# Performance work log

Measured on AMD Instinct MI355X. Metric: run time of the kernel, lower is better.

Reference implementation:

```python
import jax, jax.numpy as jnp
import numpy as np

B, D, N = 2, 256, 8192   # batch, in_channels, sequence length
CI = 128                 # inter_channels
BN_EPS = 1e-5


def conv1x1(w, b, x):
    # w: (Cout, Cin), b: (Cout,), x: (B, Cin, N) -> (B, Cout, N)
    return jnp.einsum('oc,bcn->bon', w, x) + b[None, :, None]


def maxpool2(x):
    # MaxPool1d(kernel_size=2): (B, C, N) -> (B, C, N//2)
    b, c, n = x.shape
    return x.reshape(b, c, n // 2, 2).max(axis=-1)


def setup_inputs() -> dict:
    key = jax.random.key(0)
    ks = jax.random.split(key, 11)
    s_in = 1.0 / np.sqrt(D)
    s_ci = 1.0 / np.sqrt(CI)
    return {
        'f': jax.random.normal(ks[0], (B, D, N), dtype=jnp.float32),
        'g_w': jax.random.uniform(ks[1], (CI, D), jnp.float32, -s_in, s_in),
        'g_b': jax.random.uniform(ks[2], (CI,), jnp.float32, -s_in, s_in),
        'theta_w': jax.random.uniform(ks[3], (CI, D), jnp.float32, -s_in, s_in),
        'theta_b': jax.random.uniform(ks[4], (CI,), jnp.float32, -s_in, s_in),
        'phi_w': jax.random.uniform(ks[5], (CI, D), jnp.float32, -s_in, s_in),
        'phi_b': jax.random.uniform(ks[6], (CI,), jnp.float32, -s_in, s_in),
        'W_w': jax.random.uniform(ks[7], (D, CI), jnp.float32, -s_ci, s_ci),
        'W_b': jax.random.uniform(ks[8], (D,), jnp.float32, -s_ci, s_ci),
        'bn_gamma': jax.random.normal(ks[9], (D,), dtype=jnp.float32) * 0.1,
        'bn_beta': jax.random.normal(ks[10], (D,), dtype=jnp.float32) * 0.1,
    }


def reference(f, g_w, g_b, theta_w, theta_b, phi_w, phi_b, W_w, W_b, bn_gamma, bn_beta):
    # projections (1x1 convs); g and phi are sub-sampled by maxpool(2)
    g_f = maxpool2(conv1x1(g_w, g_b, f))          # (B, CI, N/2)
    theta_f = conv1x1(theta_w, theta_b, f)        # (B, CI, N)
    phi_f = maxpool2(conv1x1(phi_w, phi_b, f))    # (B, CI, N/2)

    # affinity: theta^T @ phi, softmax over keys (no scale, as in source)
    A = jnp.einsum('bcn,bcm->bnm', theta_f, phi_f)     # (B, N, N/2)
    A = jax.nn.softmax(A, axis=-1)
    y = jnp.einsum('bnm,bcm->bcn', A, g_f)             # (B, CI, N)

    # W: 1x1 conv + BatchNorm1d (training-mode batch stats), residual
    Wy = conv1x1(W_w, W_b, y)                          # (B, D, N)
    mean = Wy.mean(axis=(0, 2), keepdims=True)
    var = Wy.var(axis=(0, 2), keepdims=True)           # biased, like torch BN
    Wy = (Wy - mean) * jax.lax.rsqrt(var + BN_EPS)
    Wy = Wy * bn_gamma[None, :, None] + bn_beta[None, :, None]
    return Wy + f
```

## Files before the change

### kernel.cpp

```cpp
#include <hip/hip_runtime.h>
#include <hip/hip_bf16.h>
#include <math.h>

#define B_ 2
#define D_ 256
#define N_ 8192
#define CI_ 128
#define M_ 4096
#define BN_EPS_ 1e-5f
#define LOG2E_ 1.4426950408889634f

#define GLOBAL_AS __attribute__((address_space(1)))
#define LDS_AS __attribute__((address_space(3)))

#define OFF_WALL 0
#define OFF_THT  65536
#define OFF_PHT  (OFF_THT + 1048576)
#define OFF_GT   (OFF_PHT + 524288)
#define OFF_YP   (OFF_GT  + 524288)
#define OFF_ML   (OFF_YP  + 4194304)
#define OFF_MEAN (OFF_ML + 131072)
#define OFF_RSTD (OFF_MEAN + 256)

typedef __attribute__((ext_vector_type(8))) short bfrag;
typedef __attribute__((ext_vector_type(4))) float f4v;
typedef __attribute__((ext_vector_type(16))) float f16v;
typedef __attribute__((ext_vector_type(4))) short s4v;
typedef __attribute__((ext_vector_type(4))) unsigned u4v;

__device__ inline unsigned short bf16rne(float x) {
    unsigned u = __float_as_uint(x);
    u += 0x7fff + ((u >> 16) & 1);
    return (unsigned short)(u >> 16);
}

__device__ inline float exp2fast(float x) {
    float r;
    asm("v_exp_f32 %0, %1" : "=v"(r) : "v"(x));
    return r;
}

__global__ __launch_bounds__(256) void wconv_kernel(
    const float* __restrict__ gw, const float* __restrict__ tw, const float* __restrict__ pw,
    const float* __restrict__ Ww, short* __restrict__ wall)
{
    int idx = blockIdx.x * 256 + threadIdx.x;
    int which = idx >> 15;
    int rem = idx & 32767;
    const float* src = (which == 0) ? gw : (which == 1) ? tw : (which == 2) ? pw : Ww;
    float v = src[rem];
    if (which == 1) v *= LOG2E_;
    wall[idx] = (short)bf16rne(v);
}

__global__ __launch_bounds__(256, 2) void proj_kernel(
    const float* __restrict__ f, const short* __restrict__ wall,
    const float* __restrict__ tb, const float* __restrict__ gb, const float* __restrict__ pb,
    short* __restrict__ th_t, short* __restrict__ g_t, short* __restrict__ ph_t)
{
    __shared__ short sF[32 * 72];

    const int tid = threadIdx.x;
    const int wave = tid >> 6, lane = tid & 63;
    const int lq = lane & 15, quad = lane >> 4;
    const int b = blockIdx.y;
    const int n0 = blockIdx.x * 32;

    const float* fb = f + (size_t)b * D_ * N_;

    f4v acc[6][2];
#pragma unroll
    for (int ct = 0; ct < 6; ct++)
#pragma unroll
        for (int nf = 0; nf < 2; nf++) acc[ct][nf] = (f4v){0.f, 0.f, 0.f, 0.f};

    const int sn = tid & 31;
    const int sgrp = tid >> 5;

    for (int kc = 0; kc < D_; kc += 64) {
        __syncthreads();
#pragma unroll
        for (int jj = 0; jj < 4; jj++) {
            int dd = kc + sgrp * 8 + 2 * jj;
            float v0 = fb[(size_t)dd * N_ + n0 + sn];
            float v1 = fb[(size_t)(dd + 1) * N_ + n0 + sn];
            unsigned pk = (unsigned)bf16rne(v0) | ((unsigned)bf16rne(v1) << 16);
            *(unsigned*)&sF[sn * 72 + sgrp * 8 + 2 * jj] = pk;
        }
        __syncthreads();

        bfrag afr[6][2], bfr[2][2];
#pragma unroll
        for (int ks = 0; ks < 2; ks++) {
#pragma unroll
            for (int nf = 0; nf < 2; nf++)
                bfr[nf][ks] = *(const bfrag*)&sF[(nf * 16 + lq) * 72 + ks * 32 + quad * 8];
#pragma unroll
            for (int ct = 0; ct < 6; ct++)
                afr[ct][ks] = *(const bfrag*)&wall[(wave * 96 + ct * 16 + lq) * 256 + kc + ks * 32 + quad * 8];
        }
#pragma unroll
        for (int ks = 0; ks < 2; ks++)
#pragma unroll
            for (int ct = 0; ct < 6; ct++) {
                acc[ct][0] = __builtin_amdgcn_mfma_f32_16x16x32_bf16(afr[ct][ks], bfr[0][ks], acc[ct][0], 0, 0, 0);
                acc[ct][1] = __builtin_amdgcn_mfma_f32_16x16x32_bf16(afr[ct][ks], bfr[1][ks], acc[ct][1], 0, 0, 0);
            }
    }

#pragma unroll
    for (int ct = 0; ct < 6; ct++) {
        const int cf = wave * 6 + ct;
#pragma unroll
        for (int nf = 0; nf < 2; nf++) {
            f4v v = acc[ct][nf];
            const int n = n0 + nf * 16 + lq;
            if (cf < 8) {
                const int cb = cf * 16 + quad * 4;
                float pl[4];
#pragma unroll
                for (int r = 0; r < 4; r++) {
                    float o = __shfl_xor(v[r], 1);
                    pl[r] = fmaxf(v[r], o) + gb[cb + r];
                }
                if (!(lq & 1)) {
                    const int m = n >> 1;
#pragma unroll
                    for (int r = 0; r < 4; r++)
                        g_t[((size_t)b * CI_ + cb + r) * M_ + m] = (short)bf16rne(pl[r]);
                }
            } else if (cf < 16) {
                const int cb = (cf - 8) * 16 + quad * 4;
                s4v o;
#pragma unroll
                for (int r = 0; r < 4; r++) o[r] = (short)bf16rne(v[r] + tb[cb + r] * LOG2E_);
                *(s4v*)&th_t[((size_t)b * N_ + n) * CI_ + cb] = o;
            } else {
                const int cb = (cf - 16) * 16 + quad * 4;
                float pl[4];
#pragma unroll
                for (int r = 0; r < 4; r++) {
                    float o = __shfl_xor(v[r], 1);
                    pl[r] = fmaxf(v[r], o) + pb[cb + r];
                }
                if (!(lq & 1)) {
                    const int m = n >> 1;
                    s4v o;
#pragma unroll
                    for (int r = 0; r < 4; r++) o[r] = (short)bf16rne(pl[r]);
                    *(s4v*)&ph_t[((size_t)b * M_ + m) * CI_ + cb] = o;
                }
            }
        }
    }
}

__global__ __launch_bounds__(256, 2) void attn_kernel(
    const short* __restrict__ th_p, const short* __restrict__ ph_p,
    const short* __restrict__ g_p, short* __restrict__ yp, float* __restrict__ ml)
{
    __shared__ short sPh[2][64 * 128];
    __shared__ short sG [2][128 * 64];

    const int tid = threadIdx.x;
    const int wave = tid >> 6, lane = tid & 63;
    const int l = lane & 31, h = lane >> 5;

    const int bid = blockIdx.x;
    const int b = bid & 1;
    const int split = (bid >> 1) & 3;
    const int q0 = (bid >> 3) * 128;
    const int qg = q0 + wave * 32 + l;

    const short* thr = th_p + ((size_t)b * N_ + qg) * CI_;
    bfrag tf[8];
#pragma unroll
    for (int s = 0; s < 8; s++)
        tf[s] = *(const bfrag*)&thr[s * 16 + h * 8];

    f16v yacc[4];
#pragma unroll
    for (int ct = 0; ct < 4; ct++)
#pragma unroll
        for (int r = 0; r < 16; r++) yacc[ct][r] = 0.f;
    float mI = -INFINITY, lI = 0.f;

    const short* phg = ph_p + (size_t)b * M_ * CI_;
    const short* gg  = g_p + (size_t)b * CI_ * M_;

    const int k0 = split * 1024;
    const int xm = l & 15;

    const int prow = (lane >> 4);
    const int pslot = lane & 15;
    const int grow = (lane >> 3);
    const int gslot = lane & 7;
    const int gcg = gslot ^ grow;

#define STAGE_DMA(BUF, KC)                                                                  \
    do {                                                                                    \
        _Pragma("unroll")                                                                   \
        for (int p = 0; p < 4; p++) {                                                       \
            const int rp = wave * 16 + p * 4 + prow;                     \
            const int cg = pslot ^ (p * 4 + prow);                   \
            __builtin_amdgcn_global_load_lds(                                               \
                (const GLOBAL_AS void*)(phg + (size_t)((KC) + rp) * 128 + cg * 8),          \
                (LDS_AS void*)(&sPh[BUF][(wave * 16 + p * 4) * 128]), 16, 0, 0);            \
        }                                                                                   \
        _Pragma("unroll")                                                                   \
        for (int p = 0; p < 4; p++) {                                                       \
            const int cp = wave * 32 + p * 8 + grow;                      \
            __builtin_amdgcn_global_load_lds(                                               \
                (const GLOBAL_AS void*)(gg + (size_t)cp * M_ + (KC) + gcg * 8),             \
                (LDS_AS void*)(&sG[BUF][(wave * 32 + p * 8) * 64]), 16, 0, 0);              \
        }                                                                                   \
    } while (0)

    STAGE_DMA(0, k0);

    int cur = 0;
    for (int kc = k0; kc < k0 + 1024; kc += 64) {
        __syncthreads();
        const bool nxt = (kc + 64 < k0 + 1024);
        if (nxt) {
            STAGE_DMA(cur ^ 1, kc + 64);
            __builtin_amdgcn_sched_barrier(0);
        }

        f16v sv[2];
        __builtin_amdgcn_s_setprio(1);
#pragma unroll
        for (int kt = 0; kt < 2; kt++) {
            f16v a;
#pragma unroll
            for (int r = 0; r < 16; r++) a[r] = 0.f;
#pragma unroll
            for (int s = 0; s < 8; s++) {
                bfrag pa = *(const bfrag*)&sPh[cur][(kt * 32 + l) * 128 + (((s << 1) | h) ^ xm) * 8];
                a = __builtin_amdgcn_mfma_f32_32x32x16_bf16(pa, tf[s], a, 0, 0, 0);
            }
            sv[kt] = a;
        }
        __builtin_amdgcn_s_setprio(0);

        float mx = fmaxf(sv[0][0], sv[1][0]);
#pragma unroll
        for (int r = 1; r < 16; r++) mx = fmaxf(mx, fmaxf(sv[0][r], sv[1][r]));
        mx = fmaxf(mx, __shfl_xor(mx, 32));

        if (__any(mx > mI + 8.f)) {
            float mnew = fmaxf(mI, mx);
            float al = exp2fast(mI - mnew);
            lI *= al;
#pragma unroll
            for (int ct = 0; ct < 4; ct++)
#pragma unroll
                for (int r = 0; r < 16; r++) yacc[ct][r] *= al;
            mI = mnew;
        }

        float ps = 0.f;
        unsigned pw[16];
#pragma unroll
        for (int kt = 0; kt < 2; kt++)
#pragma unroll
            for (int i = 0; i < 8; i++) {
                const int r = 2 * i;
                float p0 = exp2fast(sv[kt][r] - mI);
                float p1 = exp2fast(sv[kt][r + 1] - mI);
                ps += p0 + p1;
                unsigned pk;
                asm("v_cvt_pk_bf16_f32 %0, %1, %2" : "=v"(pk) : "v"(p0), "v"(p1));
                pw[kt * 8 + (i >> 1) * 2 + (i & 1)] = pk;
            }
        ps += __shfl_xor(ps, 32);
        lI += ps;

        bfrag pf[4];
#pragma unroll
        for (int s = 0; s < 4; s++) {
            const int kt = s >> 1;
            const int iA = kt * 8 + ((2 * s) & 3) * 2;
            const int iB = kt * 8 + ((2 * s + 1) & 3) * 2;
            unsigned A0 = pw[iA], A1 = pw[iA + 1];
            unsigned B0 = pw[iB], B1 = pw[iB + 1];
            unsigned O0 = h ? B0 : A0;
            unsigned O1 = h ? B1 : A1;
            unsigned Xs0 = h ? A0 : B0;
            unsigned Xs1 = h ? A1 : B1;
            unsigned X0 = (unsigned)__shfl_xor((int)Xs0, 32);
            unsigned X1 = (unsigned)__shfl_xor((int)Xs1, 32);
            u4v t;
            t.x = h ? X0 : O0;
            t.y = h ? X1 : O1;
            t.z = h ? O0 : X0;
            t.w = h ? O1 : X1;
            pf[s] = __builtin_bit_cast(bfrag, t);
        }

        __builtin_amdgcn_s_setprio(1);
#pragma unroll
        for (int ct = 0; ct < 4; ct++)
#pragma unroll
            for (int s = 0; s < 4; s++) {
                bfrag ga = *(const bfrag*)&sG[cur][(ct * 32 + l) * 64 + ((((s << 1) | h) ^ (l & 7)) * 8)];
                yacc[ct] = __builtin_amdgcn_mfma_f32_32x32x16_bf16(ga, pf[s], yacc[ct], 0, 0, 0);
            }
        __builtin_amdgcn_s_setprio(0);

        cur ^= 1;
    }
#undef STAGE_DMA

    short* yb = yp + (((size_t)split * B_ + b) * CI_) * N_;
#pragma unroll
    for (int ct = 0; ct < 4; ct++)
#pragma unroll
        for (int r = 0; r < 16; r++) {
            int c = ct * 32 + (r & 3) + 8 * (r >> 2) + 4 * h;
            yb[(size_t)c * N_ + qg] = (short)bf16rne(yacc[ct][r]);
        }
    if (h == 0) {
        float* mlb = ml + ((split * B_ + b) * 2) * N_;
        mlb[qg] = mI;
        mlb[N_ + qg] = lI;
    }
}

__global__ __launch_bounds__(256) void wy_merge_kernel(
    const short* __restrict__ yp, const float* __restrict__ ml,
    const short* __restrict__ wall2, const float* __restrict__ Wb,
    float* __restrict__ out)
{
    const int tid = threadIdx.x;
    const int wave = tid >> 6, lane = tid & 63;
    const int l = lane & 31, h = lane >> 5;
    const int b = blockIdx.y;
    const int n = blockIdx.x * 32 + l;

    float m[4], lv[4];
#pragma unroll
    for (int sp = 0; sp < 4; sp++) {
        const float* mlb = ml + ((sp * B_ + b) * 2) * N_;
        m[sp] = mlb[n];
        lv[sp] = mlb[N_ + n];
    }
    float mmax = fmaxf(fmaxf(m[0], m[1]), fmaxf(m[2], m[3]));
    float e[4], den = 0.f;
#pragma unroll
    for (int sp = 0; sp < 4; sp++) { e[sp] = exp2fast(m[sp] - mmax); den += lv[sp] * e[sp]; }
    float inv = 1.0f / den;
#pragma unroll
    for (int sp = 0; sp < 4; sp++) e[sp] *= inv;

    const unsigned short* ypu = (const unsigned short*)yp;
    bfrag by[8];
#pragma unroll
    for (int s = 0; s < 8; s++) {
#pragma unroll
        for (int j = 0; j < 8; j++) {
            const int c = s * 16 + h * 8 + j;
            float a = 0.f;
#pragma unroll
            for (int sp = 0; sp < 4; sp++) {
                unsigned short v = ypu[(((size_t)sp * B_ + b) * CI_ + c) * N_ + n];
                a = fmaf(e[sp], __uint_as_float((unsigned)v << 16), a);
            }
            by[s][j] = (short)bf16rne(a);
        }
    }

    f16v acc[2];
#pragma unroll
    for (int rt = 0; rt < 2; rt++)
#pragma unroll
        for (int r = 0; r < 16; r++) acc[rt][r] = 0.f;

#pragma unroll
    for (int s = 0; s < 8; s++)
#pragma unroll
        for (int rt = 0; rt < 2; rt++) {
            bfrag aw = *(const bfrag*)&wall2[((wave * 2 + rt) * 32 + l) * 128 + s * 16 + h * 8];
            acc[rt] = __builtin_amdgcn_mfma_f32_32x32x16_bf16(aw, by[s], acc[rt], 0, 0, 0);
        }

#pragma unroll
    for (int rt = 0; rt < 2; rt++)
#pragma unroll
        for (int r = 0; r < 16; r++) {
            const int d = (wave * 2 + rt) * 32 + (r & 3) + 8 * (r >> 2) + 4 * h;
            out[((size_t)b * D_ + d) * N_ + n] = acc[rt][r] + Wb[d];
        }
}

__global__ __launch_bounds__(256) void stats_kernel(
    const float* __restrict__ wy, float* __restrict__ mean, float* __restrict__ rstd)
{
    __shared__ float ssum[256], ssq[256];
    int d = blockIdx.x;
    int tid = threadIdx.x;
    float s = 0.f, sq = 0.f;
    for (int b = 0; b < B_; b++) {
        const float* p = wy + (size_t)b * D_ * N_ + (size_t)d * N_;
        for (int i = tid; i < N_; i += 256) {
            float v = p[i];
            s += v;
            sq = fmaf(v, v, sq);
        }
    }
    ssum[tid] = s; ssq[tid] = sq;
    __syncthreads();
    for (int st = 128; st > 0; st >>= 1) {
        if (tid < st) { ssum[tid] += ssum[tid + st]; ssq[tid] += ssq[tid + st]; }
        __syncthreads();
    }
    if (tid == 0) {
        float inv = 1.0f / (float)(B_ * N_);
        float mn = ssum[0] * inv;
        float var = ssq[0] * inv - mn * mn;
        mean[d] = mn;
        rstd[d] = rsqrtf(var + BN_EPS_);
    }
}

__global__ __launch_bounds__(256) void bn_res_kernel(
    float* __restrict__ out, const float* __restrict__ f,
    const float* __restrict__ mean, const float* __restrict__ rstd,
    const float* __restrict__ gamma, const float* __restrict__ beta)
{
    int i = blockIdx.x * 256 + threadIdx.x;
    size_t e = (size_t)i * 4;
    int d = (int)((e >> 13) & 255);
    float4 wy = ((const float4*)out)[i];
    float4 ff = ((const float4*)f)[i];
    float sc = rstd[d] * gamma[d];
    float mn = mean[d];
    float bt = beta[d];
    float4 r;
    r.x = (wy.x - mn) * sc + bt + ff.x;
    r.y = (wy.y - mn) * sc + bt + ff.y;
    r.z = (wy.z - mn) * sc + bt + ff.z;
    r.w = (wy.w - mn) * sc + bt + ff.w;
    ((float4*)out)[i] = r;
}

extern "C" void kernel_launch(void* const* d_in, const int* in_sizes, int n_in,
                              void* d_out, int out_size, void* d_ws, size_t ws_size,
                              hipStream_t stream)
{
    const float* f   = (const float*)d_in[0];
    const float* g_w = (const float*)d_in[1];
    const float* g_b = (const float*)d_in[2];
    const float* t_w = (const float*)d_in[3];
    const float* t_b = (const float*)d_in[4];
    const float* p_w = (const float*)d_in[5];
    const float* p_b = (const float*)d_in[6];
    const float* W_w = (const float*)d_in[7];
    const float* W_b = (const float*)d_in[8];
    const float* gam = (const float*)d_in[9];
    const float* bet = (const float*)d_in[10];
    float* out = (float*)d_out;
    float* ws = (float*)d_ws;

    short* wall  = (short*)(ws + OFF_WALL);
    short* wall2 = wall + 3 * 32768;
    short* th_t = (short*)(ws + OFF_THT);
    short* ph_t = (short*)(ws + OFF_PHT);
    short* g_t  = (short*)(ws + OFF_GT);
    short* ypart = (short*)(ws + OFF_YP);
    float* mlp = ws + OFF_ML;
    float* mnp = ws + OFF_MEAN;
    float* rsp = ws + OFF_RSTD;

    wconv_kernel<<<512, 256, 0, stream>>>(g_w, t_w, p_w, W_w, wall);
    proj_kernel<<<dim3(N_ / 32, B_), 256, 0, stream>>>(f, wall, t_b, g_b, p_b,
                                                       th_t, g_t, ph_t);
    attn_kernel<<<512, 256, 0, stream>>>(th_t, ph_t, g_t, ypart, mlp);
    wy_merge_kernel<<<dim3(N_ / 32, B_), 256, 0, stream>>>(ypart, mlp, wall2, W_b, out);
    stats_kernel<<<D_, 256, 0, stream>>>(out, mnp, rsp);
    bn_res_kernel<<<(B_ * D_ * N_ / 4) / 256, 256, 0, stream>>>(out, f, mnp, rsp, gam, bet);
}
```

Before: 186.3 us.

## Load G fragments directly to registers, transpose partial-y layout, vectorize merge and stats loads

The attention kernel stops staging G tiles through LDS and reads the MFMA A-fragments for G straight from global memory into registers at the top of each K step, which cuts LDS footprint and DMA traffic. Partial y outputs are now stored query-major (N x CI) as 4-wide vectors, so the merge kernel reads 16-byte chunks per split instead of scalar strided shorts, and packs to bf16 with v_cvt_pk_bf16_f32. The stats kernel switches to float4 loads. The risk is that the direct global G loads are latency-exposed and uncoalesced per lane, with no double buffering.

New measurement: 209.3 us. 12.3% more time.

```diff
diff --git a/kernel.cpp b/kernel.cpp
--- a/kernel.cpp
+++ b/kernel.cpp
@@ -160,7 +160,6 @@
     const short* __restrict__ g_p, short* __restrict__ yp, float* __restrict__ ml)
 {
     __shared__ short sPh[2][64 * 128];
-    __shared__ short sG [2][128 * 64];
 
     const int tid = threadIdx.x;
     const int wave = tid >> 6, lane = tid & 63;
@@ -193,9 +192,6 @@
 
     const int prow = (lane >> 4);
     const int pslot = lane & 15;
-    const int grow = (lane >> 3);
-    const int gslot = lane & 7;
-    const int gcg = gslot ^ grow;
 
 #define STAGE_DMA(BUF, KC)                                                                  \
     do {                                                                                    \
@@ -207,13 +203,6 @@
                 (const GLOBAL_AS void*)(phg + (size_t)((KC) + rp) * 128 + cg * 8),          \
                 (LDS_AS void*)(&sPh[BUF][(wave * 16 + p * 4) * 128]), 16, 0, 0);            \
         }                                                                                   \
-        _Pragma("unroll")                                                                   \
-        for (int p = 0; p < 4; p++) {                                                       \
-            const int cp = wave * 32 + p * 8 + grow;                      \
-            __builtin_amdgcn_global_load_lds(                                               \
-                (const GLOBAL_AS void*)(gg + (size_t)cp * M_ + (KC) + gcg * 8),             \
-                (LDS_AS void*)(&sG[BUF][(wave * 32 + p * 8) * 64]), 16, 0, 0);              \
-        }                                                                                   \
     } while (0)
 
     STAGE_DMA(0, k0);
@@ -222,10 +211,16 @@
     for (int kc = k0; kc < k0 + 1024; kc += 64) {
         __syncthreads();
         const bool nxt = (kc + 64 < k0 + 1024);
-        if (nxt) {
-            STAGE_DMA(cur ^ 1, kc + 64);
-            __builtin_amdgcn_sched_barrier(0);
-        }
+
+        bfrag ga[4][4];
+#pragma unroll
+        for (int ct = 0; ct < 4; ct++)
+#pragma unroll
+            for (int s = 0; s < 4; s++)
+                ga[ct][s] = *(const bfrag*)&gg[(size_t)(ct * 32 + l) * M_ + kc + s * 16 + h * 8];
+
+        if (nxt) STAGE_DMA(cur ^ 1, kc + 64);
+        __builtin_amdgcn_sched_barrier(0);
 
         f16v sv[2];
         __builtin_amdgcn_s_setprio(1);
@@ -302,23 +297,24 @@
 #pragma unroll
         for (int ct = 0; ct < 4; ct++)
 #pragma unroll
-            for (int s = 0; s < 4; s++) {
-                bfrag ga = *(const bfrag*)&sG[cur][(ct * 32 + l) * 64 + ((((s << 1) | h) ^ (l & 7)) * 8)];
-                yacc[ct] = __builtin_amdgcn_mfma_f32_32x32x16_bf16(ga, pf[s], yacc[ct], 0, 0, 0);
-            }
+            for (int s = 0; s < 4; s++)
+                yacc[ct] = __builtin_amdgcn_mfma_f32_32x32x16_bf16(ga[ct][s], pf[s], yacc[ct], 0, 0, 0);
         __builtin_amdgcn_s_setprio(0);
 
         cur ^= 1;
     }
 #undef STAGE_DMA
 
-    short* yb = yp + (((size_t)split * B_ + b) * CI_) * N_;
+    short* yb = yp + (((size_t)split * B_ + b) * N_) * CI_;
 #pragma unroll
     for (int ct = 0; ct < 4; ct++)
 #pragma unroll
-        for (int r = 0; r < 16; r++) {
-            int c = ct * 32 + (r & 3) + 8 * (r >> 2) + 4 * h;
-            yb[(size_t)c * N_ + qg] = (short)bf16rne(yacc[ct][r]);
+        for (int rq = 0; rq < 4; rq++) {
+            const int c0 = ct * 32 + 8 * rq + 4 * h;
+            s4v o;
+#pragma unroll
+            for (int j = 0; j < 4; j++) o[j] = (short)bf16rne(yacc[ct][rq * 4 + j]);
+            *(s4v*)&yb[(size_t)qg * CI_ + c0] = o;
         }
     if (h == 0) {
         float* mlb = ml + ((split * B_ + b) * 2) * N_;
@@ -353,21 +349,30 @@
 #pragma unroll
     for (int sp = 0; sp < 4; sp++) e[sp] *= inv;
 
-    const unsigned short* ypu = (const unsigned short*)yp;
     bfrag by[8];
 #pragma unroll
     for (int s = 0; s < 8; s++) {
-#pragma unroll
-        for (int j = 0; j < 8; j++) {
-            const int c = s * 16 + h * 8 + j;
-            float a = 0.f;
-#pragma unroll
-            for (int sp = 0; sp < 4; sp++) {
-                unsigned short v = ypu[(((size_t)sp * B_ + b) * CI_ + c) * N_ + n];
-                a = fmaf(e[sp], __uint_as_float((unsigned)v << 16), a);
+        float a[8];
+#pragma unroll
+        for (int j = 0; j < 8; j++) a[j] = 0.f;
+#pragma unroll
+        for (int sp = 0; sp < 4; sp++) {
+            bfrag yv = *(const bfrag*)&yp[(((size_t)sp * B_ + b) * N_ + n) * CI_ + s * 16 + h * 8];
+            u4v u = __builtin_bit_cast(u4v, yv);
+#pragma unroll
+            for (int p = 0; p < 4; p++) {
+                a[2 * p]     = fmaf(e[sp], __uint_as_float(u[p] << 16), a[2 * p]);
+                a[2 * p + 1] = fmaf(e[sp], __uint_as_float(u[p] & 0xffff0000u), a[2 * p + 1]);
             }
-            by[s][j] = (short)bf16rne(a);
-        }
+        }
+        u4v pk;
+#pragma unroll
+        for (int p = 0; p < 4; p++) {
+            unsigned r;
+            asm("v_cvt_pk_bf16_f32 %0, %1, %2" : "=v"(r) : "v"(a[2 * p]), "v"(a[2 * p + 1]));
+            pk[p] = r;
+        }
+        by[s] = __builtin_bit_cast(bfrag, pk);
     }
 
     f16v acc[2];
@@ -401,11 +406,14 @@
     int tid = threadIdx.x;
     float s = 0.f, sq = 0.f;
     for (int b = 0; b < B_; b++) {
-        const float* p = wy + (size_t)b * D_ * N_ + (size_t)d * N_;
-        for (int i = tid; i < N_; i += 256) {
-            float v = p[i];
-            s += v;
-            sq = fmaf(v, v, sq);
+        const float4* p = (const float4*)(wy + (size_t)b * D_ * N_ + (size_t)d * N_);
+        for (int i = tid; i < N_ / 4; i += 256) {
+            float4 v = p[i];
+            s += v.x + v.y + v.z + v.w;
+            sq = fmaf(v.x, v.x, sq);
+            sq = fmaf(v.y, v.y, sq);
+            sq = fmaf(v.z, v.z, sq);
+            sq = fmaf(v.w, v.w, sq);
         }
     }
     ssum[tid] = s; ssq[tid] = sq;
```
